# Kernel optimization log

Measured on AMD Instinct MI355X. Metric: run time of the kernel, lower is better.

The kernel has to match this reference:

```python
import jax, jax.numpy as jnp
import numpy as np

N_INST = 50
TAU = 1.0
ALPHA = 1.0


def smooth_top1_svm(logits, targets, n_classes=2):
    # SmoothTop1SVM (topk.svm): tau * logsumexp((s + alpha*(1-onehot_y))/tau) - s_y, mean over batch
    delta = ALPHA * (1.0 - jax.nn.one_hot(targets, n_classes, dtype=logits.dtype))
    lse = TAU * jax.nn.logsumexp((logits + delta) / TAU, axis=1)
    s_y = jnp.take_along_axis(logits, targets[:, None], axis=1)[:, 0]
    return jnp.mean(lse - s_y)


def setup_inputs() -> dict:
    key = jax.random.key(0)
    ks = jax.random.split(key, 14)
    N, E, L, D, C = 131072, 1024, 512, 256, 2
    g = lambda k, shp: jax.random.normal(k, shp, dtype=jnp.float32) * (shp[-1] ** -0.5)
    return {
        "x": jax.random.normal(ks[0], (N, E), dtype=jnp.float32),
        "label": 0,  # static python int: class with in-class instance eval
        "Wc": g(ks[1], (L, E)), "bc": jnp.zeros((L,), jnp.float32),
        "Wv": g(ks[2], (D, L)), "bv": jnp.zeros((D,), jnp.float32),
        "Wu": g(ks[3], (D, L)), "bu": jnp.zeros((D,), jnp.float32),
        "Wa": g(ks[4], (C, D)), "ba": jnp.zeros((C,), jnp.float32),
        "Winst": g(ks[5], (C, 2, L)), "binst": jnp.zeros((C, 2), jnp.float32),
        "Wbag": g(ks[6], (C, L)), "bbag": jnp.zeros((C,), jnp.float32),
    }


def reference(x, label, Wc, bc, Wv, bv, Wu, bu, Wa, ba, Winst, binst, Wbag, bbag):
    C = Wa.shape[0]
    # gated attention backbone
    h = jax.nn.relu(x @ Wc.T + bc)                      # [N, L] compressed features
    a = jnp.tanh(h @ Wv.T + bv)                          # [N, D]
    b = jax.nn.sigmoid(h @ Wu.T + bu)                    # [N, D]
    A = (a * b) @ Wa.T + ba                              # [N, C]
    x_att = A.T                                          # [C, N]
    raw_attention = x_att
    attn = jax.nn.softmax(x_att, axis=1)                 # [C, N]

    # instance-level eval (in-class branch only; subtyping=False skips others)
    total_loss = jnp.zeros((), jnp.float32)
    for c in range(C):
        if c == label:
            attn_c = attn[c]                             # [N]
            _, top_p = jax.lax.top_k(attn_c, N_INST)     # most attended
            _, top_n = jax.lax.top_k(-attn_c, N_INST)    # least attended
            inst = jnp.concatenate([h[top_p], h[top_n]], axis=0)   # [2*n_inst, L]
            logits_i = inst @ Winst[c].T + binst[c]                 # [2*n_inst, 2]
            targets = jnp.concatenate([jnp.ones((N_INST,), jnp.int32),
                                       jnp.zeros((N_INST,), jnp.int32)])
            total_loss = total_loss + smooth_top1_svm(logits_i, targets)

    # bag-level: multi-branch, one Linear(L,1) per class
    bag_rep = attn @ h                                   # [C, L]
    logits = (jnp.sum(bag_rep * Wbag, axis=1) + bbag)[None, :]  # [1, C]
    y_proba = jax.nn.softmax(logits, axis=1)
    return (logits, y_proba, raw_attention, total_loss)
```

## Files before the change

kernel.cpp:

```cpp
#include <hip/hip_runtime.h>
#include <hip/hip_bf16.h>
#include <math.h>

#define NROWS 131072
#define E 1024
#define L 512
#define DD 256
#define NI 50
#define CAP 2048
#define NBINS 16384

typedef __attribute__((ext_vector_type(8))) short bf16x8;
typedef __attribute__((ext_vector_type(4))) float f32x4;

__device__ __forceinline__ unsigned short f2bf(float f) {
  unsigned u = __float_as_uint(f);
  unsigned r = (u + 0x7FFFu + ((u >> 16) & 1u)) >> 16;
  return (unsigned short)r;
}
__device__ __forceinline__ float bf2f(unsigned short b) {
  return __uint_as_float(((unsigned)b) << 16);
}
__device__ __forceinline__ float frcp(float x) { return __builtin_amdgcn_rcpf(x); }
__device__ __forceinline__ float fsig(float x) { return frcp(1.0f + __expf(-x)); }
__device__ __forceinline__ float ftanh(float x) { return 2.0f * frcp(1.0f + __expf(-2.0f * x)) - 1.0f; }
__device__ __forceinline__ unsigned encf(float f) {
  unsigned u = __float_as_uint(f);
  return (u & 0x80000000u) ? ~u : (u | 0x80000000u);
}
__device__ __forceinline__ float decf(unsigned e) {
  unsigned b = (e & 0x80000000u) ? (e & 0x7FFFFFFFu) : ~e;
  return __uint_as_float(b);
}
__device__ __forceinline__ unsigned cvtpk(float a, float b) {
  unsigned r;
  asm("v_cvt_pk_bf16_f32 %0, %1, %2" : "=v"(r) : "v"(a), "v"(b));
  return r;
}

#define GLDS16(gp, lp)                                                        \
  __builtin_amdgcn_global_load_lds(                                           \
      (const __attribute__((address_space(1))) void*)(gp),                    \
      (__attribute__((address_space(3))) void*)(lp), 16, 0, 0)

__global__ void k0_init(const float* __restrict__ Wc, const float* __restrict__ Wv,
                        const float* __restrict__ Wu,
                        unsigned short* __restrict__ WcB, unsigned short* __restrict__ W2B,
                        float* __restrict__ Aws, float* __restrict__ tws,
                        unsigned* __restrict__ hist,
                        float* __restrict__ scalF, unsigned* __restrict__ scalU) {
  const int i0 = blockIdx.x * blockDim.x + threadIdx.x;
  const int str = gridDim.x * blockDim.x;
  if (i0 < 4) scalF[i0] = 0.f;
  if (i0 < 16) scalU[i0] = (i0 == 0) ? 0xFFFFFFFFu : 0u;
  for (int k = i0; k < NBINS; k += str) hist[k] = 0u;
  for (int k = i0; k < NROWS * 2; k += str) { Aws[k] = 0.f; tws[k] = 0.f; }
  for (int k = i0; k < L * E; k += str) WcB[k] = f2bf(Wc[k]);
  for (int k = i0; k < DD * L; k += str) { W2B[k] = f2bf(Wv[k]); W2B[DD * L + k] = f2bf(Wu[k]); }
}

__global__ __launch_bounds__(256) void k1_gemm1(const float* __restrict__ x,
                                                const unsigned short* __restrict__ WcB,
                                                const float* __restrict__ bc,
                                                const float* __restrict__ Wbag,
                                                unsigned short* __restrict__ hB,
                                                float* __restrict__ tws) {
  __shared__ __align__(16) float xs[2][128 * 64];
  __shared__ __align__(16) unsigned short wt[2][256 * 64];
  const int tid = threadIdx.x;
  const int lane = tid & 63;
  const int wv = tid >> 6;
  const int cbk = blockIdx.x & 1;
  const int rbk = blockIdx.x >> 1;
  const int row0 = rbk << 7;
  const int col0 = cbk << 8;
  const int wr = wv >> 1, wc = wv & 1;
  const int q = lane >> 4, c15 = lane & 15;

  f32x4 acc[4][8];
#pragma unroll
  for (int i = 0; i < 4; ++i)
#pragma unroll
    for (int j = 0; j < 8; ++j) acc[i][j] = {0.f, 0.f, 0.f, 0.f};

#define K1_STAGE(B, KK)                                                        \
  {                                                                            \
    _Pragma("unroll")                                                          \
    for (int i = 0; i < 8; ++i) {                                              \
      const int g = (wv << 3) + i;                                             \
      const int j = (g << 2) + (lane >> 4);                                    \
      const int s = lane & 15;                                                 \
      const int s4 = (s ^ (j & 15)) << 2;                                      \
      GLDS16(x + (size_t)(row0 + j) * E + (KK) + s4, &xs[B][g << 8]);          \
    }                                                                          \
    _Pragma("unroll")                                                          \
    for (int i = 0; i < 8; ++i) {                                              \
      const int g = (wv << 3) + i;                                             \
      const int slot = (g << 6) + lane;                                        \
      const int j = slot >> 3;                                                 \
      const int s = slot & 7;                                                  \
      const int k8 = s ^ (j & 7);                                              \
      GLDS16(WcB + (size_t)(col0 + j) * E + (KK) + (k8 << 3), &wt[B][g << 9]); \
    }                                                                          \
  }

  K1_STAGE(0, 0);
  __syncthreads();

  for (int t = 0; t < 16; ++t) {
    const int cur = t & 1;
    if (t < 15) K1_STAGE(cur ^ 1, (t + 1) << 6);
    const float* xsb = xs[cur];
    const unsigned short* wtb = wt[cur];
#pragma unroll
    for (int ks = 0; ks < 2; ++ks) {
      const int ch = (ks << 2) + q;
      union { bf16x8 v; unsigned u[4]; } af[4];
#pragma unroll
      for (int mt = 0; mt < 4; ++mt) {
        const int rr = (wr << 6) + (mt << 4) + c15;
        const int r15 = rr & 15;
        const f32x4 lo = *(const f32x4*)(xsb + (rr << 6) + ((((ch << 1)    ) ^ r15) << 2));
        const f32x4 hi = *(const f32x4*)(xsb + (rr << 6) + ((((ch << 1) | 1) ^ r15) << 2));
        af[mt].u[0] = cvtpk(lo[0], lo[1]);
        af[mt].u[1] = cvtpk(lo[2], lo[3]);
        af[mt].u[2] = cvtpk(hi[0], hi[1]);
        af[mt].u[3] = cvtpk(hi[2], hi[3]);
      }
#pragma unroll
      for (int nt = 0; nt < 8; ++nt) {
        const int jj = (wc << 7) + (nt << 4) + c15;
        const bf16x8 bb = *(const bf16x8*)(wtb + (jj << 6) + ((ch ^ (jj & 7)) << 3));
#pragma unroll
        for (int mt = 0; mt < 4; ++mt)
          acc[mt][nt] = __builtin_amdgcn_mfma_f32_16x16x32_bf16(af[mt].v, bb, acc[mt][nt], 0, 0, 0);
      }
    }
    __syncthreads();
  }
  float bias[8], wb0[8], wb1[8];
#pragma unroll
  for (int nt = 0; nt < 8; ++nt) {
    const int colg = col0 + (wc << 7) + (nt << 4) + c15;
    bias[nt] = bc[colg];
    wb0[nt] = Wbag[colg];
    wb1[nt] = Wbag[L + colg];
  }
#pragma unroll
  for (int mt = 0; mt < 4; ++mt) {
#pragma unroll
    for (int r = 0; r < 4; ++r) {
      const int rowg = row0 + (wr << 6) + (mt << 4) + (q << 2) + r;
      float tp0 = 0.f, tp1 = 0.f;
#pragma unroll
      for (int nt = 0; nt < 8; ++nt) {
        const int colg = col0 + (wc << 7) + (nt << 4) + c15;
        float v = acc[mt][nt][r] + bias[nt];
        v = v > 0.f ? v : 0.f;
        tp0 += v * wb0[nt];
        tp1 += v * wb1[nt];
        const unsigned short hb = f2bf(v);
        const unsigned short ob = (unsigned short)__shfl_xor((int)hb, 1, 64);
        if (!(lane & 1)) {
          *(unsigned*)(hB + (size_t)rowg * L + colg) = (unsigned)hb | ((unsigned)ob << 16);
        }
      }
#pragma unroll
      for (int off = 1; off < 16; off <<= 1) {
        tp0 += __shfl_xor(tp0, off, 64);
        tp1 += __shfl_xor(tp1, off, 64);
      }
      if (c15 == 0) {
        atomicAdd(&tws[(rowg << 1)], tp0);
        atomicAdd(&tws[(rowg << 1) + 1], tp1);
      }
    }
  }
}

__global__ __launch_bounds__(256) void k2_gemm2(const unsigned short* __restrict__ hB,
                                                const unsigned short* __restrict__ W2B,
                                                const float* __restrict__ bv,
                                                const float* __restrict__ bu,
                                                const float* __restrict__ Wa,
                                                float* __restrict__ Aws) {
  __shared__ __align__(16) unsigned short hs[2][128 * 64];
  __shared__ __align__(16) unsigned short wt[2][256 * 64];
  const int tid = threadIdx.x, lane = tid & 63, wv = tid >> 6;
  const int cbk = blockIdx.x & 1, rbk = blockIdx.x >> 1;
  const int row0 = rbk << 7;
  const int q = lane >> 4, c15 = lane & 15;

  f32x4 acc[2][16];
#pragma unroll
  for (int i = 0; i < 2; ++i)
#pragma unroll
    for (int j = 0; j < 16; ++j) acc[i][j] = {0.f, 0.f, 0.f, 0.f};

#define K2_STAGE(B, KK)                                                         \
  {                                                                             \
    _Pragma("unroll")                                                           \
    for (int i = 0; i < 4; ++i) {                                               \
      const int g = (wv << 2) + i;                                              \
      const int slot = (g << 6) + lane;                                         \
      const int j = slot >> 3;                                                  \
      const int s = slot & 7;                                                   \
      const int k8 = s ^ (j & 7);                                               \
      GLDS16(hB + (size_t)(row0 + j) * L + (KK) + (k8 << 3), &hs[B][g << 9]);   \
    }                                                                           \
    _Pragma("unroll")                                                           \
    for (int i = 0; i < 8; ++i) {                                               \
      const int g = (wv << 3) + i;                                              \
      const int slot = (g << 6) + lane;                                         \
      const int j = slot >> 3;                                                  \
      const int s = slot & 7;                                                   \
      const int k8 = s ^ (j & 7);                                               \
      const int w2row = (j < 128) ? ((cbk << 7) + j) : (DD + (cbk << 7) + (j - 128)); \
      GLDS16(W2B + (size_t)w2row * L + (KK) + (k8 << 3), &wt[B][g << 9]);       \
    }                                                                           \
  }

  K2_STAGE(0, 0);
  __syncthreads();

  for (int t = 0; t < 8; ++t) {
    const int cur = t & 1;
    if (t < 7) K2_STAGE(cur ^ 1, (t + 1) << 6);
    const unsigned short* hsb = hs[cur];
    const unsigned short* wtb = wt[cur];
#pragma unroll
    for (int ks = 0; ks < 2; ++ks) {
      const int ch = (ks << 2) + q;
      bf16x8 af[2];
#pragma unroll
      for (int mt = 0; mt < 2; ++mt) {
        const int rr = (wv << 5) + (mt << 4) + c15;
        af[mt] = *(const bf16x8*)(hsb + (rr << 6) + ((ch ^ (rr & 7)) << 3));
      }
#pragma unroll
      for (int nt = 0; nt < 16; ++nt) {
        const int jj = (nt << 4) + c15;
        const bf16x8 bb = *(const bf16x8*)(wtb + (jj << 6) + ((ch ^ (jj & 7)) << 3));
        acc[0][nt] = __builtin_amdgcn_mfma_f32_16x16x32_bf16(af[0], bb, acc[0][nt], 0, 0, 0);
        acc[1][nt] = __builtin_amdgcn_mfma_f32_16x16x32_bf16(af[1], bb, acc[1][nt], 0, 0, 0);
      }
    }
    __syncthreads();
  }
  float wa0[8], wa1[8], bvv[8], buv[8];
#pragma unroll
  for (int nt = 0; nt < 8; ++nt) {
    const int d = (cbk << 7) + (nt << 4) + c15;
    wa0[nt] = Wa[d]; wa1[nt] = Wa[DD + d];
    bvv[nt] = bv[d]; buv[nt] = bu[d];
  }
#pragma unroll
  for (int mt = 0; mt < 2; ++mt) {
#pragma unroll
    for (int r = 0; r < 4; ++r) {
      const int rowg = row0 + (wv << 5) + (mt << 4) + (q << 2) + r;
      float p0 = 0.f, p1 = 0.f;
#pragma unroll
      for (int nt = 0; nt < 8; ++nt) {
        const float av = ftanh(acc[mt][nt][r] + bvv[nt]);
        const float bx = fsig(acc[mt][nt + 8][r] + buv[nt]);
        const float ab = av * bx;
        p0 += ab * wa0[nt];
        p1 += ab * wa1[nt];
      }
#pragma unroll
      for (int off = 1; off < 16; off <<= 1) {
        p0 += __shfl_xor(p0, off, 64);
        p1 += __shfl_xor(p1, off, 64);
      }
      if (c15 == 0) {
        atomicAdd(&Aws[(rowg << 1)], p0);
        atomicAdd(&Aws[(rowg << 1) + 1], p1);
      }
    }
  }
}

__global__ void k3a_elem(const float* __restrict__ Aws, const float* __restrict__ tws,
                         const float* __restrict__ ba, const int* __restrict__ lblp,
                         float* __restrict__ out,
                         float* __restrict__ scalF, unsigned* __restrict__ scalU) {
  const int row = blockIdx.x * 256 + threadIdx.x;
  const int lane = threadIdx.x & 63;
  const float2 Ap = ((const float2*)Aws)[row];
  const float2 tp = ((const float2*)tws)[row];
  const float A0 = Ap.x + ba[0];
  const float A1 = Ap.y + ba[1];
  out[4 + row] = A0;
  out[4 + NROWS + row] = A1;
  const float e0 = __expf(A0), e1 = __expf(A1);
  float z0 = e0, z1 = e1, s0 = e0 * tp.x, s1 = e1 * tp.y;
  const int lbl = *lblp;
  unsigned u = encf(lbl ? A1 : A0);
  unsigned umin = u, umax = u;
#pragma unroll
  for (int off = 1; off < 64; off <<= 1) {
    z0 += __shfl_xor(z0, off, 64);
    z1 += __shfl_xor(z1, off, 64);
    s0 += __shfl_xor(s0, off, 64);
    s1 += __shfl_xor(s1, off, 64);
    const unsigned om = (unsigned)__shfl_xor((int)umin, off, 64);
    const unsigned oM = (unsigned)__shfl_xor((int)umax, off, 64);
    umin = umin < om ? umin : om;
    umax = umax > oM ? umax : oM;
  }
  if (lane == 0) {
    atomicAdd(&scalF[0], z0); atomicAdd(&scalF[1], z1);
    atomicAdd(&scalF[2], s0); atomicAdd(&scalF[3], s1);
    atomicMin(&scalU[0], umin);
    atomicMax(&scalU[1], umax);
  }
}

__global__ __launch_bounds__(1024) void k3b_hist(const float* __restrict__ out,
                                                 const int* __restrict__ lblp,
                                                 const unsigned* __restrict__ scalU,
                                                 unsigned* __restrict__ hist) {
  __shared__ unsigned lh[NBINS];
  const int tid = threadIdx.x;
  for (int i = tid; i < NBINS; i += 1024) lh[i] = 0u;
  __syncthreads();
  const int lbl = *lblp;
  const int row = blockIdx.x * 1024 + tid;
  const float A = out[4 + (size_t)lbl * NROWS + row];
  const float mn = decf(scalU[0]);
  const float mx = decf(scalU[1]);
  const float scale = (mx > mn) ? (float)(NBINS - 1) / (mx - mn) : 0.f;
  int bin = (int)((A - mn) * scale);
  bin = bin < 0 ? 0 : (bin > NBINS - 1 ? NBINS - 1 : bin);
  atomicAdd(&lh[bin], 1u);
  __syncthreads();
  for (int i = tid; i < NBINS; i += 1024) {
    const unsigned c = lh[i];
    if (c) atomicAdd(&hist[i], c);
  }
}

__global__ void k4_scan(const unsigned* __restrict__ hist,
                        const float* __restrict__ scalF,
                        unsigned* __restrict__ scalU,
                        const float* __restrict__ bbag,
                        float* __restrict__ out) {
  __shared__ unsigned csum[256];
  const int t = threadIdx.x;
  unsigned s = 0;
  for (int b = 0; b < 64; ++b) s += hist[t * 64 + b];
  csum[t] = s;
  __syncthreads();
  if (t == 0) {
    unsigned acc = 0; int ch = 255;
    for (; ch > 0; --ch) { if (acc + csum[ch] >= NI) break; acc += csum[ch]; }
    unsigned binHi = 0;
    for (int b = ch * 64 + 63; b >= ch * 64; --b) { acc += hist[b]; if (acc >= NI) { binHi = (unsigned)b; break; } }
    scalU[6] = binHi;
    acc = 0; int cl = 0;
    for (; cl < 255; ++cl) { if (acc + csum[cl] >= NI) break; acc += csum[cl]; }
    unsigned binLo = NBINS - 1;
    for (int b = cl * 64; b < cl * 64 + 64; ++b) { acc += hist[b]; if (acc >= NI) { binLo = (unsigned)b; break; } }
    scalU[7] = binLo;
    const float l0 = scalF[2] / scalF[0] + bbag[0];
    const float l1 = scalF[3] / scalF[1] + bbag[1];
    const float m = fmaxf(l0, l1);
    const float e0 = __expf(l0 - m), e1 = __expf(l1 - m);
    const float inv = 1.0f / (e0 + e1);
    out[0] = l0; out[1] = l1; out[2] = e0 * inv; out[3] = e1 * inv;
  }
}

__global__ void k5_collect(const float* __restrict__ out,
                           const int* __restrict__ lblp,
                           unsigned* __restrict__ scalU,
                           unsigned* __restrict__ chK, unsigned* __restrict__ chI,
                           unsigned* __restrict__ clK, unsigned* __restrict__ clI) {
  const int binHi = (int)scalU[6], binLo = (int)scalU[7];
  const float mn = decf(scalU[0]);
  const float mx = decf(scalU[1]);
  const float scale = (mx > mn) ? (float)(NBINS - 1) / (mx - mn) : 0.f;
  const int lbl = *lblp;
  const float* Ap = out + 4 + (size_t)lbl * NROWS;
  const int n = blockIdx.x * 256 + threadIdx.x;
  const float A = Ap[n];
  int bin = (int)((A - mn) * scale);
  bin = bin < 0 ? 0 : (bin > NBINS - 1 ? NBINS - 1 : bin);
  const unsigned u = encf(A);
  if (bin >= binHi) { unsigned p = atomicAdd(&scalU[4], 1u); if (p < CAP) { chK[p] = u; chI[p] = (unsigned)n; } }
  if (bin <= binLo) { unsigned p = atomicAdd(&scalU[5], 1u); if (p < CAP) { clK[p] = u; clI[p] = (unsigned)n; } }
}

__global__ __launch_bounds__(256) void k6_loss(const unsigned* __restrict__ scalU,
                                               const unsigned* __restrict__ chK, const unsigned* __restrict__ chI,
                                               const unsigned* __restrict__ clK, const unsigned* __restrict__ clI,
                                               const unsigned short* __restrict__ hB,
                                               const float* __restrict__ Winst,
                                               const float* __restrict__ binst,
                                               const int* __restrict__ lblp,
                                               float* __restrict__ out) {
  __shared__ unsigned kH[CAP], iH[CAP], kL[CAP], iL[CAP];
  __shared__ int selT[NI], selB[NI];
  __shared__ float lossA[256];
  const int t = threadIdx.x;
  const int lbl = *lblp;
  const unsigned cH = scalU[4], cL = scalU[5];
  const int nH = (int)(cH < CAP ? cH : CAP);
  const int nL = (int)(cL < CAP ? cL : CAP);
  if (t < NI) { selT[t] = 0; selB[t] = 0; }
  for (int i = t; i < nH; i += 256) { kH[i] = chK[i]; iH[i] = chI[i]; }
  for (int i = t; i < nL; i += 256) { kL[i] = clK[i]; iL[i] = clI[i]; }
  __syncthreads();
  for (int c = t; c < nH; c += 256) {
    const unsigned k = kH[c], id = iH[c];
    int rank = 0;
    for (int j = 0; j < nH; ++j) rank += (kH[j] > k) || (kH[j] == k && iH[j] < id);
    if (rank < NI) selT[rank] = (int)id;
  }
  for (int c = t; c < nL; c += 256) {
    const unsigned k = kL[c], id = iL[c];
    int rank = 0;
    for (int j = 0; j < nL; ++j) rank += (kL[j] < k) || (kL[j] == k && iL[j] < id);
    if (rank < NI) selB[rank] = (int)id;
  }
  __syncthreads();
  float loss = 0.f;
  if (t < 2 * NI) {
    const int idx = (t < NI) ? selT[t] : selB[t - NI];
    const int target = (t < NI) ? 1 : 0;
    const unsigned short* hp = hB + (size_t)idx * L;
    const float* w0 = Winst + (size_t)lbl * 2 * L;
    const float* w1 = w0 + L;
    float l0 = binst[lbl * 2 + 0], l1 = binst[lbl * 2 + 1];
    for (int k = 0; k < L; ++k) {
      const float hv = bf2f(hp[k]);
      l0 += hv * w0[k];
      l1 += hv * w1[k];
    }
    const float z0 = l0 + (target ? 1.0f : 0.0f);
    const float z1 = l1 + (target ? 0.0f : 1.0f);
    const float m = fmaxf(z0, z1);
    const float lse = m + logf(__expf(z0 - m) + __expf(z1 - m));
    loss = lse - (target ? l1 : l0);
  }
  lossA[t] = loss;
  __syncthreads();
  for (int sft = 128; sft; sft >>= 1) {
    if (t < sft) lossA[t] += lossA[t + sft];
    __syncthreads();
  }
  if (t == 0) out[4 + 2 * NROWS] = lossA[0] / 100.0f;
}

extern "C" void kernel_launch(void* const* d_in, const int* in_sizes, int n_in,
                              void* d_out, int out_size, void* d_ws, size_t ws_size,
                              hipStream_t stream) {
  const float* x     = (const float*)d_in[0];
  const int*   lbl   = (const int*)d_in[1];
  const float* Wc    = (const float*)d_in[2];
  const float* bc    = (const float*)d_in[3];
  const float* Wv    = (const float*)d_in[4];
  const float* bv    = (const float*)d_in[5];
  const float* Wu    = (const float*)d_in[6];
  const float* bu    = (const float*)d_in[7];
  const float* Wa    = (const float*)d_in[8];
  const float* ba    = (const float*)d_in[9];
  const float* Winst = (const float*)d_in[10];
  const float* binst = (const float*)d_in[11];
  const float* Wbag  = (const float*)d_in[12];
  const float* bbag  = (const float*)d_in[13];
  float* out = (float*)d_out;
  char* ws = (char*)d_ws;

  unsigned short* hB   = (unsigned short*)(ws);
  unsigned short* WcB  = (unsigned short*)(ws + 134217728LL);
  unsigned short* W2B  = (unsigned short*)(ws + 135266304LL);
  float*          Aws  = (float*)(ws + 135790592LL);
  float*          tws  = (float*)(ws + 136839168LL);
  unsigned*       hist = (unsigned*)(ws + 137887744LL);
  float*          scalF= (float*)(ws + 137953280LL);
  unsigned*       scalU= (unsigned*)(ws + 137953344LL);
  unsigned*       chK  = (unsigned*)(ws + 137953408LL);
  unsigned*       chI  = chK + CAP;
  unsigned*       clK  = chI + CAP;
  unsigned*       clI  = clK + CAP;

  k0_init<<<2048, 256, 0, stream>>>(Wc, Wv, Wu, WcB, W2B, Aws, tws, hist, scalF, scalU);
  k1_gemm1<<<2048, 256, 0, stream>>>(x, WcB, bc, Wbag, hB, tws);
  k2_gemm2<<<2048, 256, 0, stream>>>(hB, W2B, bv, bu, Wa, Aws);
  k3a_elem<<<512, 256, 0, stream>>>(Aws, tws, ba, lbl, out, scalF, scalU);
  k3b_hist<<<128, 1024, 0, stream>>>(out, lbl, scalU, hist);
  k4_scan<<<1, 256, 0, stream>>>(hist, scalF, scalU, bbag, out);
  k5_collect<<<512, 256, 0, stream>>>(out, lbl, scalU, chK, chI, clK, clI);
  k6_loss<<<1, 256, 0, stream>>>(scalU, chK, chI, clK, clI, hB, Winst, binst, lbl, out);
}
```

Before: 1.311 ms.

## Prefetch two stages ahead with partial vmcnt waits in both GEMM loops

Both GEMM main loops now issue loads for stage t+2 after the compute barrier, and each iteration waits only until the older stage's global-to-LDS loads have landed, using an explicit s_waitcnt vmcnt count instead of a full __syncthreads drain. Raw s_barrier calls are wrapped in sched_barrier fences so the compiler cannot move memory operations across them. This is meant to keep more loads in flight and overlap memory latency with MFMA work. The code depends on the hardcoded vmcnt values (16 for the first GEMM, 12 for the second) matching the exact number of loads each stage issues, so it may read stale LDS data if the compiler emits a different load count.

```diff
diff --git a/kernel.cpp b/kernel.cpp
--- a/kernel.cpp
+++ b/kernel.cpp
@@ -42,6 +42,9 @@
   __builtin_amdgcn_global_load_lds(                                           \
       (const __attribute__((address_space(1))) void*)(gp),                    \
       (__attribute__((address_space(3))) void*)(lp), 16, 0, 0)
+
+#define SBAR() __builtin_amdgcn_s_barrier()
+#define SCHED0() __builtin_amdgcn_sched_barrier(0)
 
 __global__ void k0_init(const float* __restrict__ Wc, const float* __restrict__ Wv,
                         const float* __restrict__ Wu,
@@ -105,11 +108,18 @@
   }
 
   K1_STAGE(0, 0);
-  __syncthreads();
+  K1_STAGE(1, 64);
 
   for (int t = 0; t < 16; ++t) {
     const int cur = t & 1;
-    if (t < 15) K1_STAGE(cur ^ 1, (t + 1) << 6);
+    if (t < 15) {
+      asm volatile("s_waitcnt vmcnt(16)" ::: "memory");
+    } else {
+      asm volatile("s_waitcnt vmcnt(0)" ::: "memory");
+    }
+    SCHED0();
+    SBAR();
+    SCHED0();
     const float* xsb = xs[cur];
     const unsigned short* wtb = wt[cur];
 #pragma unroll
@@ -136,7 +146,10 @@
           acc[mt][nt] = __builtin_amdgcn_mfma_f32_16x16x32_bf16(af[mt].v, bb, acc[mt][nt], 0, 0, 0);
       }
     }
-    __syncthreads();
+    SCHED0();
+    SBAR();
+    SCHED0();
+    if (t < 14) K1_STAGE(cur, (t + 2) << 6);
   }
   float bias[8], wb0[8], wb1[8];
 #pragma unroll
@@ -221,11 +234,18 @@
   }
 
   K2_STAGE(0, 0);
-  __syncthreads();
+  K2_STAGE(1, 64);
 
   for (int t = 0; t < 8; ++t) {
     const int cur = t & 1;
-    if (t < 7) K2_STAGE(cur ^ 1, (t + 1) << 6);
+    if (t < 7) {
+      asm volatile("s_waitcnt vmcnt(12)" ::: "memory");
+    } else {
+      asm volatile("s_waitcnt vmcnt(0)" ::: "memory");
+    }
+    SCHED0();
+    SBAR();
+    SCHED0();
     const unsigned short* hsb = hs[cur];
     const unsigned short* wtb = wt[cur];
 #pragma unroll
@@ -245,7 +265,10 @@
         acc[1][nt] = __builtin_amdgcn_mfma_f32_16x16x32_bf16(af[1], bb, acc[1][nt], 0, 0, 0);
       }
     }
-    __syncthreads();
+    SCHED0();
+    SBAR();
+    SCHED0();
+    if (t < 6) K2_STAGE(cur, (t + 2) << 6);
   }
   float wa0[8], wa1[8], bvv[8], buv[8];
 #pragma unroll
```

Result: faster. 1.273 ms (-2.9%).
